# Kernel optimization log

Measured on AMD Instinct MI355X. Metric: run time of the kernel, lower is better.

Reference implementation:

```python
import jax, jax.numpy as jnp
import numpy as np

GRID_SIZE, SPLINE_ORDER = 5, 3  # efficient-kan KANLinear defaults
NUM_BASES = GRID_SIZE + SPLINE_ORDER


def b_splines(x, grid):
    # x: (N, in_dim), grid: (in_dim, GRID_SIZE + 2*SPLINE_ORDER + 1)
    xe = x[..., None]
    bases = ((xe >= grid[:, :-1]) & (xe < grid[:, 1:])).astype(x.dtype)
    for k in range(1, SPLINE_ORDER + 1):  # Cox-de Boor recursion (static, 3 iters)
        left = (xe - grid[:, : -(k + 1)]) / (grid[:, k:-1] - grid[:, : -(k + 1)])
        right = (grid[:, k + 1:] - xe) / (grid[:, k + 1:] - grid[:, 1:-k])
        bases = left * bases[..., :-1] + right * bases[..., 1:]
    return bases  # (N, in_dim, NUM_BASES)


def kan_linear(x, grid, base_w, spline_w, scaler):
    # base branch: SiLU(x) @ W_base^T ; spline branch: B-spline basis @ scaled spline weights
    n = x.shape[0]
    out_dim = base_w.shape[0]
    base = jax.nn.silu(x) @ base_w.T
    bs = b_splines(x, grid).reshape(n, -1)                    # (N, in*NUM_BASES)
    sw = (spline_w * scaler[..., None]).reshape(out_dim, -1)  # (out, in*NUM_BASES)
    return base + bs @ sw.T


def setup_inputs() -> dict:
    key = jax.random.key(0)
    N, E, F, H, C, L = 50000, 500000, 128, 128, 40, 3
    ks = jax.random.split(key, 8)
    x = jax.random.normal(ks[0], (N, F), dtype=jnp.float32)
    edge_index = jax.random.randint(ks[1], (2, E), 0, N)
    # KAN grid (registered buffer in efficient-kan): uniform over [-1,1] extended by spline_order
    h_step = 2.0 / GRID_SIZE
    pts = np.arange(-SPLINE_ORDER, GRID_SIZE + SPLINE_ORDER + 1) * h_step - 1.0
    grid_mp = jnp.asarray(np.tile(pts, (F, 1)), dtype=jnp.float32)
    D = F + L * H  # skip-concat dim into output KANLinear
    grid_out = jnp.asarray(np.tile(pts, (D, 1)), dtype=jnp.float32)
    s = 0.1
    conv_base_w = jax.random.normal(ks[2], (L, H, F), dtype=jnp.float32) * s
    conv_spline_w = jax.random.normal(ks[3], (L, H, F, NUM_BASES), dtype=jnp.float32) * s
    conv_scaler = jnp.ones((L, H, F), dtype=jnp.float32)
    conv_bias = jnp.zeros((L, H), dtype=jnp.float32)
    bn_gamma = jnp.ones((L, H), dtype=jnp.float32)
    bn_beta = jnp.zeros((L, H), dtype=jnp.float32)
    out_base_w = jax.random.normal(ks[4], (C, D), dtype=jnp.float32) * s
    out_spline_w = jax.random.normal(ks[5], (C, D, NUM_BASES), dtype=jnp.float32) * s
    out_scaler = jnp.ones((C, D), dtype=jnp.float32)
    return dict(x=x, edge_index=edge_index, grid_mp=grid_mp, conv_base_w=conv_base_w,
                conv_spline_w=conv_spline_w, conv_scaler=conv_scaler, conv_bias=conv_bias,
                bn_gamma=bn_gamma, bn_beta=bn_beta, grid_out=grid_out,
                out_base_w=out_base_w, out_spline_w=out_spline_w, out_scaler=out_scaler)


def reference(x, edge_index, grid_mp, conv_base_w, conv_spline_w, conv_scaler, conv_bias,
              bn_gamma, bn_beta, grid_out, out_base_w, out_spline_w, out_scaler):
    N = x.shape[0]
    L = conv_base_w.shape[0]
    # GCN normalization with self-loops (computed once; identical each layer)
    loop = jnp.arange(N)
    src = jnp.concatenate([edge_index[0], loop])
    dst = jnp.concatenate([edge_index[1], loop])
    deg = jax.ops.segment_sum(jnp.ones_like(src, dtype=x.dtype), dst, num_segments=N)
    dinv = jnp.where(deg > 0, jax.lax.rsqrt(jnp.maximum(deg, 1.0)), 0.0)
    norm = dinv[src] * dinv[dst]  # (E+N,)
    feats = [x]
    for i in range(L):  # static layer loop
        h = kan_linear(x, grid_mp, conv_base_w[i], conv_spline_w[i], conv_scaler[i])
        # symmetric-normalized sparse aggregation (gather on src, scatter-add on dst)
        h = jax.ops.segment_sum(h[src] * norm[:, None], dst, num_segments=N) + conv_bias[i]
        # BatchNorm1d (training mode: biased batch statistics over nodes)
        mu = h.mean(axis=0)
        var = h.var(axis=0)
        x = (h - mu) * jax.lax.rsqrt(var + 1e-5) * bn_gamma[i] + bn_beta[i]
        feats.append(x)  # dropout p=0.0 is identity
    xc = jnp.concatenate(feats, axis=1)  # skip-concat: (N, F + L*H)
    logits = kan_linear(xc, grid_out, out_base_w, out_spline_w, out_scaler)
    return jax.nn.log_softmax(logits, axis=1)
```

## Files before the change

### kernel.cpp

```cpp
#include <hip/hip_runtime.h>
#include <hip/hip_bf16.h>
#include <math.h>

#define F_IN   128
#define HID    128
#define NLAYER 3
#define NCLS   40
#define DCAT   512
#define OOUT   64

typedef short s16x8 __attribute__((ext_vector_type(8)));
typedef unsigned short u16x8 __attribute__((ext_vector_type(8)));
typedef unsigned short u16x4 __attribute__((ext_vector_type(4)));
typedef float f32x4 __attribute__((ext_vector_type(4)));


static __device__ __forceinline__ float silu_f(float x) {
    return x / (1.f + __expf(-x));
}

static __device__ __forceinline__ unsigned short f2bf_rn(float f) {
    union { __hip_bfloat16 h; unsigned short u; } cv;
    cv.h = __float2bfloat16(f);
    return cv.u;
}

static __device__ __forceinline__ void lds_barrier() {
    asm volatile("s_waitcnt lgkmcnt(0)" ::: "memory");
    __builtin_amdgcn_s_barrier();
}


__global__ __launch_bounds__(256) void deg_init_kernel(int* deg, int N) {
    for (int i = blockIdx.x * blockDim.x + threadIdx.x; i < N; i += gridDim.x * blockDim.x)
        deg[i] = 1;
}

__global__ __launch_bounds__(256) void deg_count_kernel(const int* __restrict__ dst, int E, int* deg) {
    for (int i = blockIdx.x * blockDim.x + threadIdx.x; i < E; i += gridDim.x * blockDim.x)
        atomicAdd(&deg[dst[i]], 1);
}

__global__ __launch_bounds__(256) void dinv_kernel(const int* __restrict__ deg, float* dinv, int N) {
    for (int i = blockIdx.x * blockDim.x + threadIdx.x; i < N; i += gridDim.x * blockDim.x)
        dinv[i] = rsqrtf((float)deg[i]);
}

__global__ __launch_bounds__(256) void scan_reduce_kernel(const int* __restrict__ deg, int* __restrict__ bsum, int N) {
    __shared__ int sh[256];
    int t = threadIdx.x;
    int e = blockIdx.x * 256 + t;
    sh[t] = (e < N) ? deg[e] : 0;
    __syncthreads();
#pragma unroll
    for (int off = 128; off > 0; off >>= 1) {
        if (t < off) sh[t] += sh[t + off];
        __syncthreads();
    }
    if (t == 0) bsum[blockIdx.x] = sh[0];
}

__global__ __launch_bounds__(256) void scan_top_kernel(const int* __restrict__ bsum, int* __restrict__ bbase, int nsb) {
    __shared__ int sh[256];
    int t = threadIdx.x;
    int chunk = (nsb + 255) >> 8;
    int begin = t * chunk;
    int end = begin + chunk; if (end > nsb) end = nsb;
    int s = 0;
    for (int i = begin; i < end; ++i) s += bsum[i];
    sh[t] = s;
    __syncthreads();
#pragma unroll
    for (int off = 1; off < 256; off <<= 1) {
        int v = 0;
        if (t >= off) v = sh[t - off];
        __syncthreads();
        if (t >= off) sh[t] += v;
        __syncthreads();
    }
    int run = (t == 0) ? 0 : sh[t - 1];
    for (int i = begin; i < end; ++i) {
        bbase[i] = run;
        run += bsum[i];
    }
}

__global__ __launch_bounds__(256) void scan_write_kernel(const int* __restrict__ deg,
                                                         const int* __restrict__ bbase,
                                                         int* __restrict__ offs, int* __restrict__ cursor, int N) {
    __shared__ int sh[256];
    int t = threadIdx.x;
    int e = blockIdx.x * 256 + t;
    int d = (e < N) ? deg[e] : 0;
    sh[t] = d;
    __syncthreads();
#pragma unroll
    for (int off = 1; off < 256; off <<= 1) {
        int v = 0;
        if (t >= off) v = sh[t - off];
        __syncthreads();
        if (t >= off) sh[t] += v;
        __syncthreads();
    }
    int incl = sh[t] + bbase[blockIdx.x];
    int excl = incl - d;
    if (e < N) {
        offs[e] = excl;
        cursor[e] = excl;
        if (e == N - 1) offs[N] = incl;
    }
}

__global__ __launch_bounds__(256) void fill_kernel(const int* __restrict__ src, const int* __restrict__ dst,
                                                   int E, int N, int* cursor, int* __restrict__ csr) {
    int total = E + N;
    for (int i = blockIdx.x * blockDim.x + threadIdx.x; i < total; i += gridDim.x * blockDim.x) {
        if (i < E) {
            int d = dst[i];
            int p = atomicAdd(&cursor[d], 1);
            csr[p] = src[i];
        } else {
            int n = i - E;
            int p = atomicAdd(&cursor[n], 1);
            csr[p] = n;
        }
    }
}

__global__ __launch_bounds__(256) void pack_conv_mfma(const float* __restrict__ bw,
                                                      const float* __restrict__ sw,
                                                      const float* __restrict__ sc,
                                                      unsigned short* __restrict__ wpk) {
    int total = NLAYER * 9 * 4 * 8 * 64 * 8;
    for (int idx = blockIdx.x * blockDim.x + threadIdx.x; idx < total; idx += gridDim.x * blockDim.x) {
        int e    = idx & 7;
        int lane = (idx >> 3) & 63;
        int cf   = (idx >> 9) & 7;
        int kk   = (idx >> 12) & 3;
        int cc   = (idx >> 14) % 9;
        int l    = idx / (9 << 14);
        int o = cf * 16 + (lane & 15);
        int k = kk * 32 + ((lane >> 4) << 3) + e;
        float v;
        if (cc == 8) {
            v = bw[(l * 128 + o) * 128 + k];
        } else {
            int f = cc * 16 + (k >> 3);
            int j = k & 7;
            int base = (l * 128 + o) * 128 + f;
            v = sw[base * 8 + j] * sc[base];
        }
        wpk[idx] = f2bf_rn(v);
    }
}

__global__ __launch_bounds__(256) void pack_out_mfma(const float* __restrict__ bw,
                                                     const float* __restrict__ sw,
                                                     const float* __restrict__ sc,
                                                     unsigned short* __restrict__ wpk) {
    int total = 36 * 4 * 4 * 64 * 8;
    for (int idx = blockIdx.x * blockDim.x + threadIdx.x; idx < total; idx += gridDim.x * blockDim.x) {
        int e    = idx & 7;
        int lane = (idx >> 3) & 63;
        int cf   = (idx >> 9) & 3;
        int kk   = (idx >> 11) & 3;
        int gcc  = idx >> 13;
        int g = gcc / 9, cc = gcc % 9;
        int o = cf * 16 + (lane & 15);
        int k = kk * 32 + ((lane >> 4) << 3) + e;
        float v = 0.f;
        if (o < NCLS) {
            if (cc == 8) {
                int f = g * 128 + k;
                v = bw[o * DCAT + f];
            } else {
                int f = g * 128 + cc * 16 + (k >> 3);
                int j = k & 7;
                int base = o * DCAT + f;
                v = sw[base * 8 + j] * sc[base];
            }
        }
        wpk[idx] = f2bf_rn(v);
    }
}


__global__ __launch_bounds__(256) void copyx_kernel(const float* __restrict__ x, float* __restrict__ xc, int N) {
    int total = N * F_IN;
    for (int idx = blockIdx.x * blockDim.x + threadIdx.x; idx < total; idx += gridDim.x * blockDim.x) {
        int n = idx >> 7, f = idx & 127;
        xc[(size_t)n * DCAT + f] = x[idx];
    }
}

__global__ __launch_bounds__(512) void affine_init_kernel(float* scA, float* shA) {
    int i = threadIdx.x;
    scA[i] = 1.f; shA[i] = 0.f;
}

template<bool CONV, bool INIT>
__global__ __launch_bounds__(256, 2) void kan_fused_kernel(
    const float* __restrict__ xc, int in_off,
    const float* __restrict__ scA, const float* __restrict__ shA,
    const unsigned short* __restrict__ wconv,
    const unsigned short* __restrict__ wout,
    unsigned short* __restrict__ htmp,
    const float* __restrict__ dinv,
    float* __restrict__ out_acc, int N) {

    __shared__ __align__(16) char lds_phi0[16384];
    __shared__ __align__(16) char lds_phi1[16384];

    const int tid = threadIdx.x;
    const int lane = tid & 63;
    const int wave = tid >> 6;
    const int l15 = lane & 15, lg = lane >> 4;
    const int nblk = blockIdx.x * 64;

    const float g0 = -1.f - 3.f * 0.4f;
    const float invh = 1.f / 0.4f;

    const int fg = tid & 3;
    const int n0 = tid >> 2;

    f32x4 accc[4][2];
    f32x4 acco[4];
    if (CONV) {
#pragma unroll
        for (int r = 0; r < 4; ++r)
#pragma unroll
            for (int c = 0; c < 2; ++c) accc[r][c] = (f32x4)0.f;
    }
#pragma unroll
    for (int r = 0; r < 4; ++r) acco[r] = (f32x4)0.f;

    float4 xqb[2], scb[2], shb[2];
    auto ldx = [&](int cc, int slot) {
        int f0 = in_off + cc * 16 + fg * 4;
        scb[slot] = *(const float4*)(scA + f0);
        shb[slot] = *(const float4*)(shA + f0);
        int gn = nblk + n0;
        xqb[slot] = (gn < N) ? *(const float4*)(xc + (size_t)gn * DCAT + f0) : (float4){0.f,0.f,0.f,0.f};
    };

    s16x8 wc_reg[4][2];
    s16x8 wo_reg[4];
    auto loadW = [&](int cc) {
        if (CONV) {
            const unsigned short* wcb = wconv + (size_t)cc * 16384;
#pragma unroll
            for (int kk = 0; kk < 4; ++kk)
#pragma unroll
                for (int c = 0; c < 2; ++c) {
                    int cf = wave * 2 + c;
                    wc_reg[kk][c] = *(const s16x8*)(wcb + (((size_t)kk * 8 + cf) * 64 + lane) * 8);
                }
        }
        const unsigned short* wob = wout + (size_t)cc * 8192;
#pragma unroll
        for (int kk = 0; kk < 4; ++kk)
            wo_reg[kk] = *(const s16x8*)(wob + (((size_t)kk * 4 + wave) * 64 + lane) * 8);
    };

    u16x4 sreg[8];

    u16x8 pcur[4];
    auto phi_compute = [&](int ccc, int slot) {
        float xi[4] = {xqb[slot].x, xqb[slot].y, xqb[slot].z, xqb[slot].w};
        float scr[4] = {scb[slot].x, scb[slot].y, scb[slot].z, scb[slot].w};
        float shr[4] = {shb[slot].x, shb[slot].y, shb[slot].z, shb[slot].w};
        u16x4 sv;
#pragma unroll
        for (int fl = 0; fl < 4; ++fl) {
            float y = fmaf(xi[fl], scr[fl], shr[fl]);
            sv[fl] = f2bf_rn(silu_f(y));
            float t = (y - g0) * invh;
            float cf = floorf(t);
            int c = (int)cf;
            float u = t - cf;
            float um = 1.f - u;
            float u2 = u * u;
            float um2 = um * um;
            float w0 = um2 * um * (1.f / 6.f);
            float w3 = u2 * u * (1.f / 6.f);
            float w1 = fmaf(fmaf(0.5f, u, -1.f), u2, 2.f / 3.f);
            float w2 = fmaf(fmaf(-0.5f, u, 0.5f), u2, fmaf(0.5f, u, 1.f / 6.f));
            bool e[11];
#pragma unroll
            for (int v = 0; v < 11; ++v) e[v] = (c == v);
#pragma unroll
            for (int s = 0; s < 8; ++s) {
                float val = 0.f;
                val = e[s] ? w3 : val;
                val = e[s + 1] ? w2 : val;
                val = e[s + 2] ? w1 : val;
                val = e[s + 3] ? w0 : val;
                pcur[fl][s] = f2bf_rn(val);
            }
        }
        sreg[ccc] = sv;
    };

    auto write_phi = [&](char* buf) {
        int swz = (n0 & 7) << 4;
#pragma unroll
        for (int i = 0; i < 4; ++i) {
            int byte = n0 * 256 + ((fg * 64 + i * 16) ^ swz);
            *(u16x8*)(buf + byte) = pcur[i];
        }
    };

    auto write_silu = [&](char* buf) {
        int swz = (n0 & 7) << 4;
#pragma unroll
        for (int ccc = 0; ccc < 8; ++ccc) {
            int byte = n0 * 256 + (((ccc * 16 + fg * 4) * 2) ^ swz);
            *(u16x4*)(buf + byte) = sreg[ccc];
        }
    };

    auto mfma_phase = [&](const char* buf) {
#pragma unroll
        for (int kk = 0; kk < 4; ++kk) {
            const int kb = kk * 64 + lg * 16;
            s16x8 af[4];
#pragma unroll
            for (int r = 0; r < 4; ++r) {
                int n = r * 16 + l15;
                af[r] = *(const s16x8*)(buf + n * 256 + (kb ^ ((n & 7) << 4)));
            }
            if (CONV) {
#pragma unroll
                for (int c = 0; c < 2; ++c)
#pragma unroll
                    for (int r = 0; r < 4; ++r)
                        accc[r][c] = __builtin_amdgcn_mfma_f32_16x16x32_bf16(af[r], wc_reg[kk][c], accc[r][c], 0, 0, 0);
            }
#pragma unroll
            for (int r = 0; r < 4; ++r)
                acco[r] = __builtin_amdgcn_mfma_f32_16x16x32_bf16(af[r], wo_reg[kk], acco[r], 0, 0, 0);
        }
    };

    ldx(0, 0);
    phi_compute(0, 0);
    ldx(1, 1);
    loadW(0);
    write_phi(lds_phi0);
    __syncthreads();

#pragma unroll
    for (int cc = 0; cc < 9; ++cc) {
        char* cur = (cc & 1) ? lds_phi1 : lds_phi0;
        char* nxt = (cc & 1) ? lds_phi0 : lds_phi1;
        if (cc < 7) ldx(cc + 2, cc & 1);
        mfma_phase(cur);
        if (cc < 8) loadW(cc + 1);
        if (cc < 7) {
            phi_compute(cc + 1, (cc + 1) & 1);
            write_phi(nxt);
        }
        if (cc == 7) write_silu(nxt);
        if (cc < 8) lds_barrier();
    }

#pragma unroll
    for (int r = 0; r < 4; ++r) {
        int nb = nblk + r * 16 + lg * 4;
        if (CONV) {
#pragma unroll
            for (int c = 0; c < 2; ++c) {
                int o = wave * 32 + c * 16 + l15;
#pragma unroll
                for (int q = 0; q < 4; ++q) {
                    int n = nb + q;
                    if (n < N) htmp[(size_t)n * HID + o] = f2bf_rn(accc[r][c][q] * dinv[n]);
                }
            }
        }
        {
            int o = wave * 16 + l15;
            if (o < NCLS) {
#pragma unroll
                for (int q = 0; q < 4; ++q) {
                    int n = nb + q;
                    if (n < N) {
                        size_t a = (size_t)n * OOUT + o;
                        float v = acco[r][q];
                        if (!INIT) v += out_acc[a];
                        out_acc[a] = v;
                    }
                }
            }
        }
    }
}

__global__ __launch_bounds__(256) void agg_kernel(const unsigned short* __restrict__ h,
                                                  const float* __restrict__ dinv,
                                                  const int* __restrict__ offs,
                                                  const int* __restrict__ csr,
                                                  const float* __restrict__ bias,
                                                  float* __restrict__ xc, int out_off, int N) {
    int n = blockIdx.x * 4 + (threadIdx.x >> 6);
    if (n >= N) return;
    int lane = threadIdx.x & 63;
    int s = offs[n], e = offs[n + 1];
    float a0 = 0.f, a1 = 0.f, b0 = 0.f, b1 = 0.f;
    float c0 = 0.f, c1 = 0.f, d0 = 0.f, d1 = 0.f;
    int i = s;
    for (; i + 4 <= e; i += 4) {
        int v0 = csr[i], v1 = csr[i + 1], v2 = csr[i + 2], v3 = csr[i + 3];
        unsigned u0 = *(const unsigned*)(h + (size_t)v0 * HID + lane * 2);
        unsigned u1 = *(const unsigned*)(h + (size_t)v1 * HID + lane * 2);
        unsigned u2 = *(const unsigned*)(h + (size_t)v2 * HID + lane * 2);
        unsigned u3 = *(const unsigned*)(h + (size_t)v3 * HID + lane * 2);
        a0 += __uint_as_float(u0 << 16);
        a1 += __uint_as_float(u0 & 0xffff0000u);
        b0 += __uint_as_float(u1 << 16);
        b1 += __uint_as_float(u1 & 0xffff0000u);
        c0 += __uint_as_float(u2 << 16);
        c1 += __uint_as_float(u2 & 0xffff0000u);
        d0 += __uint_as_float(u3 << 16);
        d1 += __uint_as_float(u3 & 0xffff0000u);
    }
    for (; i < e; ++i) {
        int v = csr[i];
        unsigned u = *(const unsigned*)(h + (size_t)v * HID + lane * 2);
        a0 += __uint_as_float(u << 16);
        a1 += __uint_as_float(u & 0xffff0000u);
    }
    a0 += b0 + c0 + d0;
    a1 += b1 + c1 + d1;
    float dn = dinv[n];
    float2 bv = *(const float2*)(bias + lane * 2);
    float2 res = {fmaf(a0, dn, bv.x), fmaf(a1, dn, bv.y)};
    *(float2*)(xc + (size_t)n * DCAT + out_off + lane * 2) = res;
}

__global__ __launch_bounds__(128) void bn_stats_kernel(const float* __restrict__ xc, int off, int N,
                                                       float* __restrict__ bnsum, float* __restrict__ bnsq) {
    int f = threadIdx.x;
    float s = 0.f, q = 0.f;
    for (int n = blockIdx.x; n < N; n += gridDim.x) {
        float v = xc[(size_t)n * DCAT + off + f];
        s += v;
        q += v * v;
    }
    atomicAdd(&bnsum[f], s);
    atomicAdd(&bnsq[f], q);
}

__global__ __launch_bounds__(128) void bn_affine_kernel(const float* __restrict__ bnsum,
                                                        const float* __restrict__ bnsq,
                                                        const float* __restrict__ gamma,
                                                        const float* __restrict__ beta,
                                                        float* scA, float* shA, int seg_off, float invN) {
    int f = threadIdx.x;
    float mu = bnsum[f] * invN;
    float var = bnsq[f] * invN - mu * mu;
    float rs = rsqrtf(var + 1e-5f);
    float s = gamma[f] * rs;
    scA[seg_off + f] = s;
    shA[seg_off + f] = fmaf(-mu, s, beta[f]);
}

__global__ __launch_bounds__(256) void logsoftmax_kernel(const float* __restrict__ oacc,
                                                         float* __restrict__ out, int N) {
    for (int n = blockIdx.x * blockDim.x + threadIdx.x; n < N; n += gridDim.x * blockDim.x) {
        const float* row = oacc + (size_t)n * OOUT;
        float m = -1e30f;
#pragma unroll
        for (int j = 0; j < NCLS; ++j) m = fmaxf(m, row[j]);
        float s = 0.f;
#pragma unroll
        for (int j = 0; j < NCLS; ++j) s += __expf(row[j] - m);
        float lse = m + __logf(s);
        float* orow = out + (size_t)n * NCLS;
#pragma unroll
        for (int j = 0; j < NCLS; ++j) orow[j] = row[j] - lse;
    }
}


extern "C" void kernel_launch(void* const* d_in, const int* in_sizes, int n_in,
                              void* d_out, int out_size, void* d_ws, size_t ws_size,
                              hipStream_t stream) {
    const float* x            = (const float*)d_in[0];
    const int*   eidx         = (const int*)d_in[1];
    const float* conv_base_w  = (const float*)d_in[3];
    const float* conv_spline_w= (const float*)d_in[4];
    const float* conv_scaler  = (const float*)d_in[5];
    const float* conv_bias    = (const float*)d_in[6];
    const float* bn_gamma     = (const float*)d_in[7];
    const float* bn_beta      = (const float*)d_in[8];
    const float* out_base_w   = (const float*)d_in[10];
    const float* out_spline_w = (const float*)d_in[11];
    const float* out_scaler   = (const float*)d_in[12];
    float* out = (float*)d_out;

    int N = in_sizes[0] / F_IN;
    int E = in_sizes[1] / 2;
    const int* esrc = eidx;
    const int* edst = eidx + E;

    int blocks = (N + 63) / 64;
    int npad = blocks * 64;
    int nsb = (N + 255) / 256;

    char* p = (char*)d_ws;
    auto carve = [&](size_t bytes) {
        char* r = p;
        p += (bytes + 255) & ~(size_t)255;
        return r;
    };
    float* xc   = (float*)carve((size_t)N * DCAT * 4);
    unsigned short* htmp = (unsigned short*)carve((size_t)npad * HID * 2);
    float* oacc = (float*)carve((size_t)npad * OOUT * 4);
    float* dinv = (float*)carve((size_t)N * 4);
    float* bn   = (float*)carve((size_t)NLAYER * 2 * HID * 4);
    float* scA  = (float*)carve((size_t)DCAT * 4);
    float* shA  = (float*)carve((size_t)DCAT * 4);
    unsigned short* wpkc = (unsigned short*)carve((size_t)NLAYER * 9 * 128 * 128 * 2);
    unsigned short* wpko = (unsigned short*)carve((size_t)36 * 64 * 128 * 2);
    int* deg    = (int*)carve((size_t)N * 4);
    int* offs   = (int*)carve((size_t)(N + 1) * 4);
    int* cursor = (int*)carve((size_t)(N + 1) * 4);
    int* bsum   = (int*)carve((size_t)nsb * 4);
    int* bbase  = (int*)carve((size_t)nsb * 4);
    int* csr    = (int*)carve((size_t)(E + N) * 4);

    hipMemsetAsync(bn, 0, NLAYER * 2 * HID * 4, stream);

    deg_init_kernel<<<512, 256, 0, stream>>>(deg, N);
    deg_count_kernel<<<1024, 256, 0, stream>>>(edst, E, deg);
    dinv_kernel<<<512, 256, 0, stream>>>(deg, dinv, N);
    scan_reduce_kernel<<<nsb, 256, 0, stream>>>(deg, bsum, N);
    scan_top_kernel<<<1, 256, 0, stream>>>(bsum, bbase, nsb);
    scan_write_kernel<<<nsb, 256, 0, stream>>>(deg, bbase, offs, cursor, N);
    fill_kernel<<<1024, 256, 0, stream>>>(esrc, edst, E, N, cursor, csr);

    pack_conv_mfma<<<1024, 256, 0, stream>>>(conv_base_w, conv_spline_w, conv_scaler, wpkc);
    pack_out_mfma<<<1024, 256, 0, stream>>>(out_base_w, out_spline_w, out_scaler, wpko);
    copyx_kernel<<<2048, 256, 0, stream>>>(x, xc, N);
    affine_init_kernel<<<1, 512, 0, stream>>>(scA, shA);

    float invN = 1.f / (float)N;
    for (int l = 0; l < NLAYER; ++l) {
        int in_off = l * HID;
        int out_off = (l + 1) * HID;
        const unsigned short* wl = wpkc + (size_t)l * 9 * 16384;
        const unsigned short* wo = wpko + (size_t)l * 9 * 8192;
        if (l == 0)
            kan_fused_kernel<true, true><<<blocks, 256, 0, stream>>>(
                xc, in_off, scA, shA, wl, wo, htmp, dinv, oacc, N);
        else
            kan_fused_kernel<true, false><<<blocks, 256, 0, stream>>>(
                xc, in_off, scA, shA, wl, wo, htmp, dinv, oacc, N);
        agg_kernel<<<(N + 3) / 4, 256, 0, stream>>>(htmp, dinv, offs, csr, conv_bias + l * HID, xc, out_off, N);
        float* bnsum = bn + l * 2 * HID;
        float* bnsq  = bnsum + HID;
        bn_stats_kernel<<<256, 128, 0, stream>>>(xc, out_off, N, bnsum, bnsq);
        bn_affine_kernel<<<1, 128, 0, stream>>>(bnsum, bnsq, bn_gamma + l * HID, bn_beta + l * HID,
                                                scA, shA, out_off, invN);
    }

    kan_fused_kernel<false, false><<<blocks, 256, 0, stream>>>(
        xc, 384, scA, shA, nullptr, wpko + (size_t)3 * 9 * 8192, htmp, dinv, oacc, N);

    logsoftmax_kernel<<<(N + 255) / 256, 256, 0, stream>>>(oacc, out, N);
}
```

Measured before the change: 537.3 us.

## Fuse BatchNorm statistics into aggregation, read input directly, and raise MFMA priority

The separate BatchNorm statistics pass is removed. The aggregation kernel now builds per-block sums and sums of squares in shared memory, writes them out as partials, and a small finalize kernel reduces those partials into the scale and shift. The copy of x into the concatenated buffer is dropped, and layer 0 reads x directly through a new stride parameter. The aggregation loop now gathers 8 neighbours per step with 16 nodes per 1024-thread block, and the MFMA phase is wrapped in s_setprio. This removes one strided full read of each layer's output and one copy pass, at the cost of shared-memory atomics and a partial-sum buffer.

After: 554.5 us. 3.2% more time.

```diff
diff --git a/kernel.cpp b/kernel.cpp
--- a/kernel.cpp
+++ b/kernel.cpp
@@ -185,14 +185,6 @@
 }
 
 
-__global__ __launch_bounds__(256) void copyx_kernel(const float* __restrict__ x, float* __restrict__ xc, int N) {
-    int total = N * F_IN;
-    for (int idx = blockIdx.x * blockDim.x + threadIdx.x; idx < total; idx += gridDim.x * blockDim.x) {
-        int n = idx >> 7, f = idx & 127;
-        xc[(size_t)n * DCAT + f] = x[idx];
-    }
-}
-
 __global__ __launch_bounds__(512) void affine_init_kernel(float* scA, float* shA) {
     int i = threadIdx.x;
     scA[i] = 1.f; shA[i] = 0.f;
@@ -200,7 +192,7 @@
 
 template<bool CONV, bool INIT>
 __global__ __launch_bounds__(256, 2) void kan_fused_kernel(
-    const float* __restrict__ xc, int in_off,
+    const float* __restrict__ xin, int xstride, int in_off,
     const float* __restrict__ scA, const float* __restrict__ shA,
     const unsigned short* __restrict__ wconv,
     const unsigned short* __restrict__ wout,
@@ -240,7 +232,8 @@
         scb[slot] = *(const float4*)(scA + f0);
         shb[slot] = *(const float4*)(shA + f0);
         int gn = nblk + n0;
-        xqb[slot] = (gn < N) ? *(const float4*)(xc + (size_t)gn * DCAT + f0) : (float4){0.f,0.f,0.f,0.f};
+        xqb[slot] = (gn < N) ? *(const float4*)(xin + (size_t)gn * xstride + f0 - in_off + (CONV ? in_off : in_off) - (xstride == F_IN ? in_off : 0))
+                             : (float4){0.f, 0.f, 0.f, 0.f};
     };
 
     s16x8 wc_reg[4][2];
@@ -320,6 +313,7 @@
     };
 
     auto mfma_phase = [&](const char* buf) {
+        __builtin_amdgcn_s_setprio(1);
 #pragma unroll
         for (int kk = 0; kk < 4; ++kk) {
             const int kb = kk * 64 + lg * 16;
@@ -340,6 +334,7 @@
             for (int r = 0; r < 4; ++r)
                 acco[r] = __builtin_amdgcn_mfma_f32_16x16x32_bf16(af[r], wo_reg[kk], acco[r], 0, 0, 0);
         }
+        __builtin_amdgcn_s_setprio(0);
     };
 
     ldx(0, 0);
@@ -396,73 +391,96 @@
     }
 }
 
-__global__ __launch_bounds__(256) void agg_kernel(const unsigned short* __restrict__ h,
-                                                  const float* __restrict__ dinv,
-                                                  const int* __restrict__ offs,
-                                                  const int* __restrict__ csr,
-                                                  const float* __restrict__ bias,
-                                                  float* __restrict__ xc, int out_off, int N) {
-    int n = blockIdx.x * 4 + (threadIdx.x >> 6);
-    if (n >= N) return;
-    int lane = threadIdx.x & 63;
-    int s = offs[n], e = offs[n + 1];
-    float a0 = 0.f, a1 = 0.f, b0 = 0.f, b1 = 0.f;
-    float c0 = 0.f, c1 = 0.f, d0 = 0.f, d1 = 0.f;
-    int i = s;
-    for (; i + 4 <= e; i += 4) {
-        int v0 = csr[i], v1 = csr[i + 1], v2 = csr[i + 2], v3 = csr[i + 3];
-        unsigned u0 = *(const unsigned*)(h + (size_t)v0 * HID + lane * 2);
-        unsigned u1 = *(const unsigned*)(h + (size_t)v1 * HID + lane * 2);
-        unsigned u2 = *(const unsigned*)(h + (size_t)v2 * HID + lane * 2);
-        unsigned u3 = *(const unsigned*)(h + (size_t)v3 * HID + lane * 2);
-        a0 += __uint_as_float(u0 << 16);
-        a1 += __uint_as_float(u0 & 0xffff0000u);
-        b0 += __uint_as_float(u1 << 16);
-        b1 += __uint_as_float(u1 & 0xffff0000u);
-        c0 += __uint_as_float(u2 << 16);
-        c1 += __uint_as_float(u2 & 0xffff0000u);
-        d0 += __uint_as_float(u3 << 16);
-        d1 += __uint_as_float(u3 & 0xffff0000u);
-    }
-    for (; i < e; ++i) {
-        int v = csr[i];
-        unsigned u = *(const unsigned*)(h + (size_t)v * HID + lane * 2);
-        a0 += __uint_as_float(u << 16);
-        a1 += __uint_as_float(u & 0xffff0000u);
-    }
-    a0 += b0 + c0 + d0;
-    a1 += b1 + c1 + d1;
-    float dn = dinv[n];
-    float2 bv = *(const float2*)(bias + lane * 2);
-    float2 res = {fmaf(a0, dn, bv.x), fmaf(a1, dn, bv.y)};
-    *(float2*)(xc + (size_t)n * DCAT + out_off + lane * 2) = res;
-}
-
-__global__ __launch_bounds__(128) void bn_stats_kernel(const float* __restrict__ xc, int off, int N,
-                                                       float* __restrict__ bnsum, float* __restrict__ bnsq) {
-    int f = threadIdx.x;
-    float s = 0.f, q = 0.f;
-    for (int n = blockIdx.x; n < N; n += gridDim.x) {
-        float v = xc[(size_t)n * DCAT + off + f];
-        s += v;
-        q += v * v;
-    }
-    atomicAdd(&bnsum[f], s);
-    atomicAdd(&bnsq[f], q);
-}
-
-__global__ __launch_bounds__(128) void bn_affine_kernel(const float* __restrict__ bnsum,
-                                                        const float* __restrict__ bnsq,
-                                                        const float* __restrict__ gamma,
-                                                        const float* __restrict__ beta,
-                                                        float* scA, float* shA, int seg_off, float invN) {
-    int f = threadIdx.x;
-    float mu = bnsum[f] * invN;
-    float var = bnsq[f] * invN - mu * mu;
-    float rs = rsqrtf(var + 1e-5f);
-    float s = gamma[f] * rs;
-    scA[seg_off + f] = s;
-    shA[seg_off + f] = fmaf(-mu, s, beta[f]);
+__global__ __launch_bounds__(1024) void agg_kernel(const unsigned short* __restrict__ h,
+                                                   const float* __restrict__ dinv,
+                                                   const int* __restrict__ offs,
+                                                   const int* __restrict__ csr,
+                                                   const float* __restrict__ bias,
+                                                   float* __restrict__ xc, int out_off,
+                                                   float4* __restrict__ partial, int N) {
+    __shared__ float4 bins[64];
+    int t = threadIdx.x;
+    int lane = t & 63;
+    if (t < 64) bins[t] = (float4){0.f, 0.f, 0.f, 0.f};
+    __syncthreads();
+
+    int n = blockIdx.x * 16 + (t >> 6);
+    if (n < N) {
+        int s = offs[n], e = offs[n + 1];
+        float s0[8], s1[8];
+#pragma unroll
+        for (int k = 0; k < 8; ++k) { s0[k] = 0.f; s1[k] = 0.f; }
+        int i = s;
+        for (; i + 8 <= e; i += 8) {
+            int vv[8];
+#pragma unroll
+            for (int k = 0; k < 8; ++k) vv[k] = csr[i + k];
+            unsigned uu[8];
+#pragma unroll
+            for (int k = 0; k < 8; ++k) uu[k] = *(const unsigned*)(h + (size_t)vv[k] * HID + lane * 2);
+#pragma unroll
+            for (int k = 0; k < 8; ++k) {
+                s0[k] += __uint_as_float(uu[k] << 16);
+                s1[k] += __uint_as_float(uu[k] & 0xffff0000u);
+            }
+        }
+        for (; i < e; ++i) {
+            int v = csr[i];
+            unsigned u = *(const unsigned*)(h + (size_t)v * HID + lane * 2);
+            s0[0] += __uint_as_float(u << 16);
+            s1[0] += __uint_as_float(u & 0xffff0000u);
+        }
+        float a0 = ((s0[0] + s0[1]) + (s0[2] + s0[3])) + ((s0[4] + s0[5]) + (s0[6] + s0[7]));
+        float a1 = ((s1[0] + s1[1]) + (s1[2] + s1[3])) + ((s1[4] + s1[5]) + (s1[6] + s1[7]));
+        float dn = dinv[n];
+        float2 bv = *(const float2*)(bias + lane * 2);
+        float x0 = fmaf(a0, dn, bv.x);
+        float x1 = fmaf(a1, dn, bv.y);
+        *(float2*)(xc + (size_t)n * DCAT + out_off + lane * 2) = (float2){x0, x1};
+        atomicAdd(&bins[lane].x, x0);
+        atomicAdd(&bins[lane].y, x1);
+        atomicAdd(&bins[lane].z, x0 * x0);
+        atomicAdd(&bins[lane].w, x1 * x1);
+    }
+    __syncthreads();
+    if (t < 64) partial[(size_t)blockIdx.x * 64 + t] = bins[t];
+}
+
+__global__ __launch_bounds__(256) void bn_finalize_kernel(const float4* __restrict__ partial, int nblk,
+                                                          const float* __restrict__ gamma,
+                                                          const float* __restrict__ beta,
+                                                          float* scA, float* shA, int seg_off, float invN) {
+    __shared__ float4 sh[256];
+    int p = blockIdx.x, t = threadIdx.x;
+    float4 acc = {0.f, 0.f, 0.f, 0.f};
+    for (int b = t; b < nblk; b += 256) {
+        float4 v = partial[(size_t)b * 64 + p];
+        acc.x += v.x; acc.y += v.y; acc.z += v.z; acc.w += v.w;
+    }
+    sh[t] = acc;
+    __syncthreads();
+#pragma unroll
+    for (int off = 128; off > 0; off >>= 1) {
+        if (t < off) {
+            sh[t].x += sh[t + off].x; sh[t].y += sh[t + off].y;
+            sh[t].z += sh[t + off].z; sh[t].w += sh[t + off].w;
+        }
+        __syncthreads();
+    }
+    if (t == 0) {
+        float4 v = sh[0];
+        int f0 = 2 * p, f1 = 2 * p + 1;
+        float mu0 = v.x * invN, mu1 = v.y * invN;
+        float var0 = v.z * invN - mu0 * mu0;
+        float var1 = v.w * invN - mu1 * mu1;
+        float rs0 = rsqrtf(var0 + 1e-5f);
+        float rs1 = rsqrtf(var1 + 1e-5f);
+        float sc0 = gamma[f0] * rs0, sc1 = gamma[f1] * rs1;
+        scA[seg_off + f0] = sc0;
+        scA[seg_off + f1] = sc1;
+        shA[seg_off + f0] = fmaf(-mu0, sc0, beta[f0]);
+        shA[seg_off + f1] = fmaf(-mu1, sc1, beta[f1]);
+    }
 }
 
 __global__ __launch_bounds__(256) void logsoftmax_kernel(const float* __restrict__ oacc,
@@ -507,6 +525,7 @@
     int blocks = (N + 63) / 64;
     int npad = blocks * 64;
     int nsb = (N + 255) / 256;
+    int nab = (N + 15) / 16;
 
     char* p = (char*)d_ws;
     auto carve = [&](size_t bytes) {
@@ -518,7 +537,7 @@
     unsigned short* htmp = (unsigned short*)carve((size_t)npad * HID * 2);
     float* oacc = (float*)carve((size_t)npad * OOUT * 4);
     float* dinv = (float*)carve((size_t)N * 4);
-    float* bn   = (float*)carve((size_t)NLAYER * 2 * HID * 4);
+    float4* partial = (float4*)carve((size_t)nab * 64 * 16);
     float* scA  = (float*)carve((size_t)DCAT * 4);
     float* shA  = (float*)carve((size_t)DCAT * 4);
     unsigned short* wpkc = (unsigned short*)carve((size_t)NLAYER * 9 * 128 * 128 * 2);
@@ -530,8 +549,6 @@
     int* bbase  = (int*)carve((size_t)nsb * 4);
     int* csr    = (int*)carve((size_t)(E + N) * 4);
 
-    hipMemsetAsync(bn, 0, NLAYER * 2 * HID * 4, stream);
-
     deg_init_kernel<<<512, 256, 0, stream>>>(deg, N);
     deg_count_kernel<<<1024, 256, 0, stream>>>(edst, E, deg);
     dinv_kernel<<<512, 256, 0, stream>>>(deg, dinv, N);
@@ -542,7 +559,6 @@
 
     pack_conv_mfma<<<1024, 256, 0, stream>>>(conv_base_w, conv_spline_w, conv_scaler, wpkc);
     pack_out_mfma<<<1024, 256, 0, stream>>>(out_base_w, out_spline_w, out_scaler, wpko);
-    copyx_kernel<<<2048, 256, 0, stream>>>(x, xc, N);
     affine_init_kernel<<<1, 512, 0, stream>>>(scA, shA);
 
     float invN = 1.f / (float)N;
@@ -553,20 +569,18 @@
         const unsigned short* wo = wpko + (size_t)l * 9 * 8192;
         if (l == 0)
             kan_fused_kernel<true, true><<<blocks, 256, 0, stream>>>(
-                xc, in_off, scA, shA, wl, wo, htmp, dinv, oacc, N);
+                x, F_IN, 0, scA, shA, wl, wo, htmp, dinv, oacc, N);
         else
             kan_fused_kernel<true, false><<<blocks, 256, 0, stream>>>(
-                xc, in_off, scA, shA, wl, wo, htmp, dinv, oacc, N);
-        agg_kernel<<<(N + 3) / 4, 256, 0, stream>>>(htmp, dinv, offs, csr, conv_bias + l * HID, xc, out_off, N);
-        float* bnsum = bn + l * 2 * HID;
-        float* bnsq  = bnsum + HID;
-        bn_stats_kernel<<<256, 128, 0, stream>>>(xc, out_off, N, bnsum, bnsq);
-        bn_affine_kernel<<<1, 128, 0, stream>>>(bnsum, bnsq, bn_gamma + l * HID, bn_beta + l * HID,
-                                                scA, shA, out_off, invN);
+                xc, DCAT, in_off, scA, shA, wl, wo, htmp, dinv, oacc, N);
+        agg_kernel<<<nab, 1024, 0, stream>>>(htmp, dinv, offs, csr, conv_bias + l * HID,
+                                             xc, out_off, partial, N);
+        bn_finalize_kernel<<<64, 256, 0, stream>>>(partial, nab, bn_gamma + l * HID, bn_beta + l * HID,
+                                                   scA, shA, out_off, invN);
     }
 
     kan_fused_kernel<false, false><<<blocks, 256, 0, stream>>>(
-        xc, 384, scA, shA, nullptr, wpko + (size_t)3 * 9 * 8192, htmp, dinv, oacc, N);
+        xc, DCAT, 384, scA, shA, nullptr, wpko + (size_t)3 * 9 * 8192, htmp, dinv, oacc, N);
 
     logsoftmax_kernel<<<(N + 255) / 256, 256, 0, stream>>>(oacc, out, N);
 }
```
